# Performance work log

Measured on AMD Instinct MI355X. Metric: run time of the kernel, lower is better.

The kernel has to match this reference:

```python
import jax, jax.numpy as jnp
import numpy as np

VOCAB = 32002        # len(tokenizer) + 2
N_HIDDEN = 512
N_COND = 1024
MAX_LENGTH = 15
BATCH = 256


def setup_inputs() -> dict:
    key = jax.random.key(0)
    ks = jax.random.split(key, 12)
    s = 0.02
    return {
        "caption": jax.random.randint(ks[0], (BATCH, 1), 0, VOCAB, dtype=jnp.int64) if jax.config.jax_enable_x64 else jax.random.randint(ks[0], (BATCH, 1), 0, VOCAB, dtype=jnp.int32),
        "img": jax.random.normal(ks[1], (BATCH, N_COND), dtype=jnp.float32),
        "embedding": jax.random.normal(ks[2], (VOCAB, N_HIDDEN), dtype=jnp.float32) * s,
        "W_cond": jax.random.normal(ks[3], (N_HIDDEN, N_COND), dtype=jnp.float32) * s,
        "b_cond": jnp.zeros((N_HIDDEN,), dtype=jnp.float32),
        "w_ih": jax.random.normal(ks[4], (3 * N_HIDDEN, N_HIDDEN), dtype=jnp.float32) * s,
        "w_hh": jax.random.normal(ks[5], (3 * N_HIDDEN, N_HIDDEN), dtype=jnp.float32) * s,
        "b_ih": jnp.zeros((3 * N_HIDDEN,), dtype=jnp.float32),
        "b_hh": jnp.zeros((3 * N_HIDDEN,), dtype=jnp.float32),
        "W_pred": jax.random.normal(ks[6], (VOCAB, N_HIDDEN), dtype=jnp.float32) * s,
        "b_pred": jnp.zeros((VOCAB,), dtype=jnp.float32),
    }


def gru_cell(x, h, w_ih, w_hh, b_ih, b_hh):
    # PyTorch GRUCell math: gates ordered (reset, update, new)
    gi = x @ w_ih.T + b_ih   # [B, 3H]
    gh = h @ w_hh.T + b_hh   # [B, 3H]
    i_r, i_z, i_n = jnp.split(gi, 3, axis=-1)
    h_r, h_z, h_n = jnp.split(gh, 3, axis=-1)
    r = jax.nn.sigmoid(i_r + h_r)
    z = jax.nn.sigmoid(i_z + h_z)
    n = jnp.tanh(i_n + r * h_n)
    return (1.0 - z) * n + z * h


def reference(caption, img, embedding, W_cond, b_cond, w_ih, w_hh, b_ih, b_hh, W_pred, b_pred):
    h0 = img @ W_cond.T + b_cond           # [B, H] initial GRU hidden state
    tok0 = caption[:, 0].astype(jnp.int32)  # seed token

    def step(carry, _):
        h, tok = carry
        x = embedding[tok]                              # [B, H] gather
        h_new = gru_cell(x, h, w_ih, w_hh, b_ih, b_hh)  # [B, H]
        logits = h_new @ W_pred.T + b_pred              # [B, V]
        nxt = jnp.argmax(logits, axis=-1).astype(jnp.int32)  # top-1 == topk(1)
        return (h_new, nxt), nxt

    (_, _), toks = jax.lax.scan(step, (h0, tok0), None, length=MAX_LENGTH - 1)
    # toks: [T-1, B] -> predictions [B, T] with seed token in column 0
    preds = jnp.concatenate([tok0[:, None], toks.T], axis=1)
    return preds
```

## Files before the change

### kernel.cpp

```cpp
#include <hip/hip_runtime.h>
#include <math.h>

#define BATCH 256
#define NH 512
#define NCOND 1024
#define NV 32002
#define NT 15
#define NVT_F32 501
#define NVT_MF  251

#define SP_P  4096256
#define SP_IH 196608
#define SP_HH 196608
#define SP_C  131072
#define SPLIT_W_BLOCKS 16001
#define SPLIT_S_BLOCKS 2048

typedef short short8 __attribute__((ext_vector_type(8)));
typedef float float4v __attribute__((ext_vector_type(4)));

__device__ __forceinline__ void async_load16(const void* g, void* l){
  __builtin_amdgcn_global_load_lds(
      (const __attribute__((address_space(1))) void*)g,
      (__attribute__((address_space(3))) void*)l, 16, 0, 0);
}

__device__ __forceinline__ void split2(float x, unsigned short& hi, unsigned short& lo){
  unsigned u = __float_as_uint(x);
  unsigned r = u + 0x7fffu + ((u >> 16) & 1u);
  hi = (unsigned short)(r >> 16);
  float fh = __uint_as_float(r & 0xffff0000u);
  float res = x - fh;
  unsigned u2 = __float_as_uint(res);
  unsigned r2 = u2 + 0x7fffu + ((u2 >> 16) & 1u);
  lo = (unsigned short)(r2 >> 16);
}

__device__ __forceinline__ unsigned long long pack_key(float v, int idx){
  unsigned u = __float_as_uint(v);
  u = (u & 0x80000000u) ? ~u : (u | 0x80000000u);
  return ((unsigned long long)u << 32) | (unsigned)(0x7fffffff - idx);
}
__device__ __forceinline__ int key_tok(unsigned long long k){
  return 0x7fffffff - (int)(unsigned)(k & 0xffffffffu);
}

__global__ void k_seed(const int* __restrict__ cap, int* __restrict__ preds){
  int b = threadIdx.x;
  preds[b*NT + 0] = cap[b];
}

__global__ __launch_bounds__(256) void k_split_w(const float* __restrict__ Wp,
    unsigned short* __restrict__ Whi, unsigned short* __restrict__ Wlo){
  size_t i = (size_t)blockIdx.x * 256 + threadIdx.x;
  float4 v = *(const float4*)(Wp + i*4);
  unsigned short h0,l0,h1,l1,h2,l2,h3,l3;
  split2(v.x,h0,l0); split2(v.y,h1,l1); split2(v.z,h2,l2); split2(v.w,h3,l3);
  ushort4 hs = {h0,h1,h2,h3};
  ushort4 ls = {l0,l1,l2,l3};
  *(ushort4*)(Whi + i*4) = hs;
  *(ushort4*)(Wlo + i*4) = ls;
}

__global__ __launch_bounds__(256) void k_split_small(
    const float* __restrict__ wih, const float* __restrict__ whh,
    const float* __restrict__ Wc,
    unsigned short* __restrict__ W6hi, unsigned short* __restrict__ W6lo,
    unsigned short* __restrict__ Wchi, unsigned short* __restrict__ Wclo){
  size_t i = (size_t)blockIdx.x * 256 + threadIdx.x;
  const float* src; unsigned short *dh, *dl; size_t off;
  if (i < SP_IH){ src = wih; dh = W6hi; dl = W6lo; off = i; }
  else if (i < SP_IH + SP_HH){
    src = whh; dh = W6hi + 786432; dl = W6lo + 786432; off = i - SP_IH;
  } else { src = Wc; dh = Wchi; dl = Wclo; off = i - SP_IH - SP_HH; }
  float4 v = *(const float4*)(src + off*4);
  unsigned short h0,l0,h1,l1,h2,l2,h3,l3;
  split2(v.x,h0,l0); split2(v.y,h1,l1); split2(v.z,h2,l2); split2(v.w,h3,l3);
  ushort4 hs = {h0,h1,h2,h3};
  ushort4 ls = {l0,l1,l2,l3};
  *(ushort4*)(dh + off*4) = hs;
  *(ushort4*)(dl + off*4) = ls;
}

__global__ __launch_bounds__(256) void k_h0_mf(
    const float* __restrict__ img,
    const unsigned short* __restrict__ Wchi, const unsigned short* __restrict__ Wclo,
    const float* __restrict__ bc,
    float* __restrict__ h0,
    unsigned short* __restrict__ hhi, unsigned short* __restrict__ hlo){
  __shared__ __align__(16) unsigned short sA[2][16*64];
  __shared__ __align__(16) unsigned short sB[2][64*64];
  int tid = threadIdx.x, w = tid >> 6, lane = tid & 63;
  int jbase = blockIdx.x * 16, bbase = blockIdx.y * 64;
  int r16 = lane & 15, q = lane >> 4;
  float4v acc = {0.f,0.f,0.f,0.f};
  for (int k0 = 0; k0 < NCOND; k0 += 64){
    {
      int arr = w >> 1, t = w & 1;
      int a = t*8 + (lane >> 3);
      int p = (lane & 7) ^ (lane >> 3);
      const unsigned short* gs = (arr ? Wclo : Wchi) + (size_t)(jbase + a)*NCOND + k0 + p*8;
      async_load16(gs, (char*)&sA[arr][0] + t*1024);
    }
    #pragma unroll
    for (int i = 0; i < 2; i++){
      int u = tid + 256*i;
      int b = u >> 3, s = u & 7;
      int p = s ^ (b & 7);
      const float* gp = img + (size_t)(bbase + b)*NCOND + k0 + p*8;
      float4 f0 = *(const float4*)gp, f1 = *(const float4*)(gp + 4);
      short8 hv, lv; unsigned short hh, ll;
      split2(f0.x,hh,ll); hv[0]=(short)hh; lv[0]=(short)ll;
      split2(f0.y,hh,ll); hv[1]=(short)hh; lv[1]=(short)ll;
      split2(f0.z,hh,ll); hv[2]=(short)hh; lv[2]=(short)ll;
      split2(f0.w,hh,ll); hv[3]=(short)hh; lv[3]=(short)ll;
      split2(f1.x,hh,ll); hv[4]=(short)hh; lv[4]=(short)ll;
      split2(f1.y,hh,ll); hv[5]=(short)hh; lv[5]=(short)ll;
      split2(f1.z,hh,ll); hv[6]=(short)hh; lv[6]=(short)ll;
      split2(f1.w,hh,ll); hv[7]=(short)hh; lv[7]=(short)ll;
      *(short8*)((char*)&sB[0][0] + b*128 + s*16) = hv;
      *(short8*)((char*)&sB[1][0] + b*128 + s*16) = lv;
    }
    __syncthreads();
    int rb = w*16 + r16;
    #pragma unroll
    for (int kh = 0; kh < 2; kh++){
      int pa = kh*4 + q;
      int offA = r16*128 + ((pa ^ (r16 & 7))*16);
      int offB = rb*128 + ((pa ^ (rb & 7))*16);
      short8 ah = *(const short8*)((const char*)&sA[0][0] + offA);
      short8 al = *(const short8*)((const char*)&sA[1][0] + offA);
      short8 bh = *(const short8*)((const char*)&sB[0][0] + offB);
      short8 bl = *(const short8*)((const char*)&sB[1][0] + offB);
      acc = __builtin_amdgcn_mfma_f32_16x16x32_bf16(ah, bh, acc, 0,0,0);
      acc = __builtin_amdgcn_mfma_f32_16x16x32_bf16(ah, bl, acc, 0,0,0);
      acc = __builtin_amdgcn_mfma_f32_16x16x32_bf16(al, bh, acc, 0,0,0);
    }
    __syncthreads();
  }
  int b = bbase + w*16 + r16;
  #pragma unroll
  for (int reg = 0; reg < 4; reg++){
    int j = jbase + q*4 + reg;
    float val = acc[reg] + bc[j];
    h0[(size_t)b*NH + j] = val;
    unsigned short sh, sl; split2(val, sh, sl);
    hhi[(size_t)b*NH + j] = sh;
    hlo[(size_t)b*NH + j] = sl;
  }
}

__global__ __launch_bounds__(256) void k_gru_mf(
    const int* __restrict__ cap,
    const unsigned long long* __restrict__ slot_prev,
    const float* __restrict__ emb,
    const unsigned short* __restrict__ W6hi, const unsigned short* __restrict__ W6lo,
    const unsigned short* __restrict__ Hhi, const unsigned short* __restrict__ Hlo,
    const float* __restrict__ bih, const float* __restrict__ bhh,
    const float* __restrict__ hprev, float* __restrict__ hnew,
    unsigned short* __restrict__ nhhi, unsigned short* __restrict__ nhlo,
    int* __restrict__ preds, int use_caption, int pred_col){
  __shared__ __align__(16) unsigned short sAh[96*128];
  __shared__ __align__(16) unsigned short sAl[96*128];
  __shared__ __align__(16) unsigned short sXh[32*128];
  __shared__ __align__(16) unsigned short sXl[32*128];
  __shared__ __align__(16) unsigned short sHh[32*128];
  __shared__ __align__(16) unsigned short sHl[32*128];
  __shared__ float comb[2][768];
  __shared__ int tok[32];
  int tid = threadIdx.x, w = tid >> 6, lane = tid & 63;
  int jbase = blockIdx.x * 16, bbase = blockIdx.y * 32;
  int bsub = w & 1, grp = w >> 1;
  int b16 = lane & 15, q = lane >> 4;

  if (tid < 32){
    int t;
    if (use_caption) t = cap[bbase + tid];
    else {
      t = key_tok(slot_prev[bbase + tid]);
      if (blockIdx.x == 0) preds[(bbase + tid)*NT + pred_col] = t;
    }
    tok[tid] = t;
  }
  __syncthreads();
  int tr0 = tok[tid >> 4];
  int tr1 = tok[16 + (tid >> 4)];

  float4v acc[3];
  #pragma unroll
  for (int g = 0; g < 3; g++) acc[g] = (float4v){0.f,0.f,0.f,0.f};

  for (int k0 = 0; k0 < NH; k0 += 128){
    #pragma unroll
    for (int i = 0; i < 12; i++){
      int idx = w*12 + i;
      int arr = idx >= 24, t = arr ? (idx - 24) : idx;
      int row = t*4 + (lane >> 4);
      int glocal = row >> 4, jr = row & 15;
      int slot = (lane & 15) ^ (row & 15);
      const unsigned short* gs = (arr ? W6lo : W6hi)
          + (size_t)(glocal*512 + jbase + jr)*NH + k0 + slot*8;
      async_load16(gs, (char*)(arr ? sAl : sAh) + t*1024);
    }
    #pragma unroll
    for (int i = 0; i < 4; i++){
      int idx = w*4 + i;
      int arr = idx >= 8, t = idx & 7;
      int row = t*4 + (lane >> 4);
      int slot = (lane & 15) ^ (row & 15);
      const unsigned short* gs = (arr ? Hlo : Hhi)
          + (size_t)(bbase + row)*NH + k0 + slot*8;
      async_load16(gs, (char*)(arr ? sHl : sHh) + t*1024);
    }
    #pragma unroll
    for (int i = 0; i < 2; i++){
      int u = tid + 256*i;
      int row = u >> 4, slot = u & 15;
      int phys = slot ^ (row & 15);
      int tr = i ? tr1 : tr0;
      const float* gp = emb + (size_t)tr*NH + k0 + slot*8;
      float4 f0 = *(const float4*)gp, f1 = *(const float4*)(gp + 4);
      short8 hv, lv; unsigned short hh, ll;
      split2(f0.x,hh,ll); hv[0]=(short)hh; lv[0]=(short)ll;
      split2(f0.y,hh,ll); hv[1]=(short)hh; lv[1]=(short)ll;
      split2(f0.z,hh,ll); hv[2]=(short)hh; lv[2]=(short)ll;
      split2(f0.w,hh,ll); hv[3]=(short)hh; lv[3]=(short)ll;
      split2(f1.x,hh,ll); hv[4]=(short)hh; lv[4]=(short)ll;
      split2(f1.y,hh,ll); hv[5]=(short)hh; lv[5]=(short)ll;
      split2(f1.z,hh,ll); hv[6]=(short)hh; lv[6]=(short)ll;
      split2(f1.w,hh,ll); hv[7]=(short)hh; lv[7]=(short)ll;
      *(short8*)((char*)sXh + row*256 + phys*16) = hv;
      *(short8*)((char*)sXl + row*256 + phys*16) = lv;
    }
    __syncthreads();
    #pragma unroll
    for (int kh = 0; kh < 4; kh++){
      int phys = (kh*4 + q) ^ b16;
      int boff = (bsub*16 + b16)*256 + phys*16;
      short8 bh = grp ? *(const short8*)((const char*)sHh + boff)
                      : *(const short8*)((const char*)sXh + boff);
      short8 bl = grp ? *(const short8*)((const char*)sHl + boff)
                      : *(const short8*)((const char*)sXl + boff);
      #pragma unroll
      for (int gi = 0; gi < 3; gi++){
        int row = (grp*3 + gi)*16 + b16;
        int aoff = row*256 + phys*16;
        short8 ah = *(const short8*)((const char*)sAh + aoff);
        short8 al = *(const short8*)((const char*)sAl + aoff);
        acc[gi] = __builtin_amdgcn_mfma_f32_16x16x32_bf16(ah, bh, acc[gi], 0,0,0);
        acc[gi] = __builtin_amdgcn_mfma_f32_16x16x32_bf16(ah, bl, acc[gi], 0,0,0);
        acc[gi] = __builtin_amdgcn_mfma_f32_16x16x32_bf16(al, bh, acc[gi], 0,0,0);
      }
    }
    __syncthreads();
  }

  if (grp == 1){
    #pragma unroll
    for (int gi = 0; gi < 3; gi++)
      #pragma unroll
      for (int reg = 0; reg < 4; reg++)
        comb[bsub][gi*256 + b16*16 + q*4 + reg] = acc[gi][reg];
  }
  __syncthreads();
  if (grp == 0){
    int b = bbase + bsub*16 + b16;
    #pragma unroll
    for (int reg = 0; reg < 4; reg++){
      int jl = q*4 + reg;
      int j = jbase + jl;
      float hr = comb[bsub][0*256 + b16*16 + jl];
      float hz = comb[bsub][1*256 + b16*16 + jl];
      float hn = comb[bsub][2*256 + b16*16 + jl];
      float gr = acc[0][reg] + hr + bih[j] + bhh[j];
      float gz = acc[1][reg] + hz + bih[j+NH] + bhh[j+NH];
      float in_ = acc[2][reg] + bih[j+2*NH];
      float hn_ = hn + bhh[j+2*NH];
      float r = 1.f/(1.f + expf(-gr));
      float z = 1.f/(1.f + expf(-gz));
      float n = tanhf(in_ + r*hn_);
      float hp = hprev[(size_t)b*NH + j];
      float val = (1.f - z)*n + z*hp;
      hnew[(size_t)b*NH + j] = val;
      unsigned short sh, sl; split2(val, sh, sl);
      nhhi[(size_t)b*NH + j] = sh;
      nhlo[(size_t)b*NH + j] = sl;
    }
  }
}

__global__ __launch_bounds__(256) void k_pred_mf(
    const unsigned short* __restrict__ Hhi, const unsigned short* __restrict__ Hlo,
    const unsigned short* __restrict__ Whi, const unsigned short* __restrict__ Wlo,
    const float* __restrict__ bp,
    unsigned long long* __restrict__ slot){
  __shared__ __align__(16) unsigned short sAh[128*64];
  __shared__ __align__(16) unsigned short sAl[128*64];
  __shared__ __align__(16) unsigned short sBh[128*64];
  __shared__ __align__(16) unsigned short sBl[128*64];
  __shared__ float sval[256];
  __shared__ int   sidx[256];
  int tid = threadIdx.x, w = tid >> 6, lane = tid & 63;
  int vt = blockIdx.x, vbase = vt*128, bbase = blockIdx.y*128;
  int mhalf = w & 1, nhalf = w >> 1;
  unsigned short* mybuf = (w==0)?sAh:(w==1)?sAl:(w==2)?sBh:sBl;
  const unsigned short* gsrc = (w==0)?Whi:(w==1)?Wlo:(w==2)?Hhi:Hlo;
  int rowbase = (w < 2) ? vbase : bbase;
  int isA = (w < 2);
  int rl = lane >> 3, sl = lane & 7;
  int pq = sl ^ rl;
  float4v acc[4][4];
  #pragma unroll
  for (int mi=0;mi<4;mi++)
    #pragma unroll
    for (int ni=0;ni<4;ni++) acc[mi][ni] = (float4v){0.f,0.f,0.f,0.f};
  int q = lane >> 4, b16 = lane & 15;

  for (int k0 = 0; k0 < NH; k0 += 64){
    #pragma unroll
    for (int t = 0; t < 16; t++){
      int grow = rowbase + t*8 + rl;
      if (isA && grow > NV-1) grow = NV-1;
      const unsigned short* gp = gsrc + (size_t)grow*NH + k0 + pq*8;
      async_load16(gp, (char*)mybuf + t*1024);
    }
    __syncthreads();
    #pragma unroll
    for (int kh = 0; kh < 2; kh++){
      int pa = kh*4 + q;
      short8 ah[4], al[4], bh[4], bl[4];
      #pragma unroll
      for (int mi=0;mi<4;mi++){
        int r = mhalf*64 + mi*16 + b16;
        int off = r*128 + ((pa ^ (r & 7))*16);
        ah[mi] = *(const short8*)((const char*)sAh + off);
        al[mi] = *(const short8*)((const char*)sAl + off);
      }
      #pragma unroll
      for (int ni=0;ni<4;ni++){
        int r = nhalf*64 + ni*16 + b16;
        int off = r*128 + ((pa ^ (r & 7))*16);
        bh[ni] = *(const short8*)((const char*)sBh + off);
        bl[ni] = *(const short8*)((const char*)sBl + off);
      }
      #pragma unroll
      for (int mi=0;mi<4;mi++)
        #pragma unroll
        for (int ni=0;ni<4;ni++){
          acc[mi][ni] = __builtin_amdgcn_mfma_f32_16x16x32_bf16(ah[mi], bh[ni], acc[mi][ni], 0,0,0);
          acc[mi][ni] = __builtin_amdgcn_mfma_f32_16x16x32_bf16(ah[mi], bl[ni], acc[mi][ni], 0,0,0);
          acc[mi][ni] = __builtin_amdgcn_mfma_f32_16x16x32_bf16(al[mi], bh[ni], acc[mi][ni], 0,0,0);
        }
    }
    __syncthreads();
  }

  float bestv[4] = {-INFINITY,-INFINITY,-INFINITY,-INFINITY};
  int   besti[4] = {0x7fffffff,0x7fffffff,0x7fffffff,0x7fffffff};
  #pragma unroll
  for (int mi=0;mi<4;mi++){
    #pragma unroll
    for (int reg=0;reg<4;reg++){
      int v = vbase + mhalf*64 + mi*16 + q*4 + reg;
      if (v < NV){
        float bpv = bp[v];
        #pragma unroll
        for (int ni=0;ni<4;ni++){
          float cand = acc[mi][ni][reg] + bpv;
          if (cand > bestv[ni] || (cand == bestv[ni] && v < besti[ni])){
            bestv[ni] = cand; besti[ni] = v;
          }
        }
      }
    }
  }
  #pragma unroll
  for (int ni=0;ni<4;ni++){
    #pragma unroll
    for (int off=16; off<=32; off<<=1){
      float ov = __shfl_xor(bestv[ni], off);
      int   oi = __shfl_xor(besti[ni], off);
      if (ov > bestv[ni] || (ov == bestv[ni] && oi < besti[ni])){
        bestv[ni] = ov; besti[ni] = oi;
      }
    }
    if (lane < 16){
      sval[w*64 + ni*16 + b16] = bestv[ni];
      sidx[w*64 + ni*16 + b16] = besti[ni];
    }
  }
  __syncthreads();
  if (tid < 128){
    int nh = tid >> 6;
    int wA = nh*2, wB = nh*2 + 1;
    int slotid = tid & 63;
    float vA = sval[wA*64 + slotid], vB = sval[wB*64 + slotid];
    int   iA = sidx[wA*64 + slotid], iB = sidx[wB*64 + slotid];
    bool takeB = (vB > vA) || (vB == vA && iB < iA);
    float bv = takeB ? vB : vA;
    int   bi = takeB ? iB : iA;
    atomicMax(slot + bbase + tid, pack_key(bv, bi));
  }
}

__global__ void k_fin_slot(const unsigned long long* __restrict__ slot,
                           int* __restrict__ preds){
  int b = threadIdx.x;
  preds[b*NT + (NT-1)] = key_tok(slot[b]);
}

__global__ __launch_bounds__(256) void k_h0_fb(const float* __restrict__ img,
                                            const float* __restrict__ Wc,
                                            const float* __restrict__ bc,
                                            float* __restrict__ h0){
  __shared__ float As[64*36];
  __shared__ float Bs[64*36];
  int tid = threadIdx.x;
  int tx = tid & 15, ty = tid >> 4;
  int jbase = blockIdx.x * 64;
  int bbase = blockIdx.y * 64;
  int lrow = tid >> 3;
  int lc4  = (tid & 7) << 2;
  float acc[4][4] = {};
  for (int k0 = 0; k0 < NCOND; k0 += 32){
    #pragma unroll
    for (int rr = 0; rr < 64; rr += 32){
      *(float4*)&As[(lrow+rr)*36 + lc4] =
          *(const float4*)(img + (size_t)(bbase+lrow+rr)*NCOND + k0 + lc4);
      *(float4*)&Bs[(lrow+rr)*36 + lc4] =
          *(const float4*)(Wc + (size_t)(jbase+lrow+rr)*NCOND + k0 + lc4);
    }
    __syncthreads();
    #pragma unroll
    for (int kk = 0; kk < 32; kk += 4){
      float4 a[4], w[4];
      #pragma unroll
      for (int i=0;i<4;i++) a[i] = *(float4*)&As[(ty+16*i)*36+kk];
      #pragma unroll
      for (int j=0;j<4;j++) w[j] = *(float4*)&Bs[(tx+16*j)*36+kk];
      #pragma unroll
      for (int i=0;i<4;i++)
        #pragma unroll
        for (int j=0;j<4;j++)
          acc[i][j] += a[i].x*w[j].x + a[i].y*w[j].y + a[i].z*w[j].z + a[i].w*w[j].w;
    }
    __syncthreads();
  }
  #pragma unroll
  for (int i=0;i<4;i++){
    int b = bbase + ty + 16*i;
    #pragma unroll
    for (int j=0;j<4;j++){
      int jj = jbase + tx + 16*j;
      h0[(size_t)b*NH + jj] = acc[i][j] + bc[jj];
    }
  }
}

__global__ __launch_bounds__(256) void k_pred_f32(const float* __restrict__ h,
                                              const float* __restrict__ Wp,
                                              const float* __restrict__ bp,
                                              float* __restrict__ pval,
                                              int* __restrict__ pidx){
  __shared__ float As[64*36];
  __shared__ float Bs[64*36];
  __shared__ float rv[64*16];
  __shared__ int   ri[64*16];
  int tid = threadIdx.x;
  int tx = tid & 15, ty = tid >> 4;
  int vt = blockIdx.x;
  int vbase = vt * 64;
  int bbase = blockIdx.y * 64;
  int lrow = tid >> 3;
  int lc4  = (tid & 7) << 2;
  float acc[4][4] = {};
  for (int k0 = 0; k0 < NH; k0 += 32){
    #pragma unroll
    for (int rr = 0; rr < 64; rr += 32){
      *(float4*)&As[(lrow+rr)*36 + lc4] =
          *(const float4*)(h + (size_t)(bbase+lrow+rr)*NH + k0 + lc4);
      int v = vbase + lrow + rr;
      float4 wv = make_float4(0.f,0.f,0.f,0.f);
      if (v < NV) wv = *(const float4*)(Wp + (size_t)v*NH + k0 + lc4);
      *(float4*)&Bs[(lrow+rr)*36 + lc4] = wv;
    }
    __syncthreads();
    #pragma unroll
    for (int kk = 0; kk < 32; kk += 4){
      float4 a[4], wv[4];
      #pragma unroll
      for (int i=0;i<4;i++) a[i] = *(float4*)&As[(ty+16*i)*36+kk];
      #pragma unroll
      for (int j=0;j<4;j++) wv[j] = *(float4*)&Bs[(tx+16*j)*36+kk];
      #pragma unroll
      for (int i=0;i<4;i++)
        #pragma unroll
        for (int j=0;j<4;j++)
          acc[i][j] += a[i].x*wv[j].x + a[i].y*wv[j].y + a[i].z*wv[j].z + a[i].w*wv[j].w;
    }
    __syncthreads();
  }
  #pragma unroll
  for (int i=0;i<4;i++){
    int bl = ty + 16*i;
    float best = -INFINITY; int bidx = 0;
    #pragma unroll
    for (int j=0;j<4;j++){
      int v = vbase + tx + 16*j;
      if (v < NV){
        float val = acc[i][j] + bp[v];
        if (val > best){ best = val; bidx = v; }
      }
    }
    rv[bl*16+tx] = best; ri[bl*16+tx] = bidx;
  }
  __syncthreads();
  if (tid < 64){
    float best = -INFINITY; int bidx = 0;
    #pragma unroll
    for (int t=0;t<16;t++){
      float v = rv[tid*16+t];
      if (v > best){ best = v; bidx = ri[tid*16+t]; }
    }
    pval[vt*BATCH + bbase + tid] = best;
    pidx[vt*BATCH + bbase + tid] = bidx;
  }
}

__global__ __launch_bounds__(256) void k_gru_fb(const int* __restrict__ cap,
    const float* __restrict__ pval, const int* __restrict__ pidx,
    const float* __restrict__ emb,
    const float* __restrict__ wih, const float* __restrict__ whh,
    const float* __restrict__ bih, const float* __restrict__ bhh,
    const float* __restrict__ hprev, float* __restrict__ hnew,
    int* __restrict__ preds, int use_caption, int pred_col, int nvt){
  __shared__ int   s_tok[32];
  __shared__ float rav[32*8];
  __shared__ int   rai[32*8];
  __shared__ float xs[32*36];
  __shared__ float hs[32*36];
  __shared__ float wis[3*16*36];
  __shared__ float whs[3*16*36];
  int tid = threadIdx.x;
  int tx = tid & 15, ty = tid >> 4;
  int jbase = blockIdx.x * 16;
  int bbase = blockIdx.y * 32;

  if (use_caption){
    if (tid < 32) s_tok[tid] = cap[bbase + tid];
  } else {
    int bl = tid >> 3, l8 = tid & 7;
    float best = -INFINITY; int bidx = 0x7fffffff;
    for (int p = l8; p < nvt; p += 8){
      float v = pval[p*BATCH + bbase + bl];
      int   i = pidx[p*BATCH + bbase + bl];
      if (v > best || (v == best && i < bidx)){ best = v; bidx = i; }
    }
    rav[bl*8 + l8] = best; rai[bl*8 + l8] = bidx;
    __syncthreads();
    if (tid < 32){
      float bb = -INFINITY; int bi = 0x7fffffff;
      #pragma unroll
      for (int t=0;t<8;t++){
        float v = rav[tid*8+t]; int i = rai[tid*8+t];
        if (v > bb || (v == bb && i < bi)){ bb = v; bi = i; }
      }
      s_tok[tid] = bi;
      if (blockIdx.x == 0) preds[(bbase+tid)*NT + pred_col] = bi;
    }
  }
  __syncthreads();

  float acc[2][6] = {};
  int lrow = tid >> 3;
  int lc4  = (tid & 7) << 2;
  for (int k0 = 0; k0 < NH; k0 += 32){
    int tokr = s_tok[lrow];
    *(float4*)&xs[lrow*36 + lc4] =
        *(const float4*)(emb + (size_t)tokr*NH + k0 + lc4);
    *(float4*)&hs[lrow*36 + lc4] =
        *(const float4*)(hprev + (size_t)(bbase+lrow)*NH + k0 + lc4);
    #pragma unroll
    for (int qy = tid; qy < 768; qy += 256){
      int g  = qy >> 7;
      int r  = (qy >> 3) & 15;
      int cc = (qy & 7) << 2;
      const float* wsrc = (g < 3) ? wih : whh;
      int gg = (g < 3) ? g : (g - 3);
      float* dst = (g < 3) ? wis : whs;
      *(float4*)&dst[gg*576 + r*36 + cc] =
          *(const float4*)(wsrc + (size_t)(gg*NH + jbase + r)*NH + k0 + cc);
    }
    __syncthreads();
    #pragma unroll
    for (int kk = 0; kk < 32; kk += 4){
      float4 x0 = *(float4*)&xs[ty*36+kk];
      float4 x1 = *(float4*)&xs[(ty+16)*36+kk];
      float4 h0v = *(float4*)&hs[ty*36+kk];
      float4 h1v = *(float4*)&hs[(ty+16)*36+kk];
      #pragma unroll
      for (int g=0; g<3; g++){
        float4 wi4 = *(float4*)&wis[g*576 + tx*36 + kk];
        float4 wh4 = *(float4*)&whs[g*576 + tx*36 + kk];
        acc[0][g]   += x0.x*wi4.x + x0.y*wi4.y + x0.z*wi4.z + x0.w*wi4.w;
        acc[1][g]   += x1.x*wi4.x + x1.y*wi4.y + x1.z*wi4.z + x1.w*wi4.w;
        acc[0][3+g] += h0v.x*wh4.x + h0v.y*wh4.y + h0v.z*wh4.z + h0v.w*wh4.w;
        acc[1][3+g] += h1v.x*wh4.x + h1v.y*wh4.y + h1v.z*wh4.z + h1v.w*wh4.w;
      }
    }
    __syncthreads();
  }
  int j = jbase + tx;
  float bi_r = bih[j], bi_z = bih[j+NH], bi_n = bih[j+2*NH];
  float bh_r = bhh[j], bh_z = bhh[j+NH], bh_n = bhh[j+2*NH];
  #pragma unroll
  for (int i=0;i<2;i++){
    int b = bbase + ty + 16*i;
    float r = 1.f/(1.f + expf(-((acc[i][0]+bi_r) + (acc[i][3]+bh_r))));
    float z = 1.f/(1.f + expf(-((acc[i][1]+bi_z) + (acc[i][4]+bh_z))));
    float n = tanhf((acc[i][2]+bi_n) + r*(acc[i][5]+bh_n));
    float hp = hprev[(size_t)b*NH + j];
    hnew[(size_t)b*NH + j] = (1.f - z)*n + z*hp;
  }
}

__global__ void k_fin(const float* __restrict__ pval, const int* __restrict__ pidx,
                      int* __restrict__ preds, int col, int nvt){
  __shared__ float rav[32*8];
  __shared__ int   rai[32*8];
  int tid = threadIdx.x;
  int bbase = blockIdx.x * 32;
  int bl = tid >> 3, l8 = tid & 7;
  float best = -INFINITY; int bidx = 0x7fffffff;
  for (int p = l8; p < nvt; p += 8){
    float v = pval[p*BATCH + bbase + bl];
    int   i = pidx[p*BATCH + bbase + bl];
    if (v > best || (v == best && i < bidx)){ best = v; bidx = i; }
  }
  rav[bl*8+l8] = best; rai[bl*8+l8] = bidx;
  __syncthreads();
  if (tid < 32){
    float bb = -INFINITY; int bi = 0x7fffffff;
    #pragma unroll
    for (int t=0;t<8;t++){
      float v = rav[tid*8+t]; int i = rai[tid*8+t];
      if (v > bb || (v == bb && i < bi)){ bb = v; bi = i; }
    }
    preds[(bbase+tid)*NT + col] = bi;
  }
}

extern "C" void kernel_launch(void* const* d_in, const int* in_sizes, int n_in,
                              void* d_out, int out_size, void* d_ws, size_t ws_size,
                              hipStream_t stream){
  const int*   cap = (const int*)d_in[0];
  const float* img = (const float*)d_in[1];
  const float* emb = (const float*)d_in[2];
  const float* Wc  = (const float*)d_in[3];
  const float* bc  = (const float*)d_in[4];
  const float* wih = (const float*)d_in[5];
  const float* whh = (const float*)d_in[6];
  const float* bih = (const float*)d_in[7];
  const float* bhh = (const float*)d_in[8];
  const float* Wp  = (const float*)d_in[9];
  const float* bp  = (const float*)d_in[10];
  int* preds = (int*)d_out;

  char* p = (char*)d_ws;
  float* h0b = (float*)p;                   p += (size_t)BATCH*NH*4;
  float* h1b = (float*)p;                   p += (size_t)BATCH*NH*4;
  float* pval = (float*)p;                  p += (size_t)NVT_F32*BATCH*4;
  int*   pidx = (int*)p;                    p += (size_t)NVT_F32*BATCH*4;
  unsigned short* Hhi0 = (unsigned short*)p; p += (size_t)BATCH*NH*2;
  unsigned short* Hlo0 = (unsigned short*)p; p += (size_t)BATCH*NH*2;
  unsigned short* Hhi1 = (unsigned short*)p; p += (size_t)BATCH*NH*2;
  unsigned short* Hlo1 = (unsigned short*)p; p += (size_t)BATCH*NH*2;
  unsigned short* Whi = (unsigned short*)p;  p += (size_t)NV*NH*2;
  unsigned short* Wlo = (unsigned short*)p;  p += (size_t)NV*NH*2;
  unsigned short* W6hi = (unsigned short*)p; p += (size_t)3072*NH*2;
  unsigned short* W6lo = (unsigned short*)p; p += (size_t)3072*NH*2;
  unsigned short* Wchi = (unsigned short*)p; p += (size_t)NH*NCOND*2;
  unsigned short* Wclo = (unsigned short*)p; p += (size_t)NH*NCOND*2;
  unsigned long long* slots = (unsigned long long*)p; p += (size_t)NT*BATCH*8;
  size_t need = (size_t)(p - (char*)d_ws);

  bool use_mfma = (ws_size >= need);

  k_seed<<<1, 256, 0, stream>>>(cap, preds);
  float* hb[2] = {h0b, h1b};

  if (use_mfma){
    hipMemsetAsync(slots, 0, (size_t)NT*BATCH*8, stream);
    k_split_small<<<dim3(SPLIT_S_BLOCKS), 256, 0, stream>>>(wih, whh, Wc,
                                                            W6hi, W6lo, Wchi, Wclo);
    k_h0_mf<<<dim3(NH/16, BATCH/64), 256, 0, stream>>>(img, Wchi, Wclo, bc,
                                                       h0b, Hhi0, Hlo0);
    unsigned short* Hhs[2] = {Hhi0, Hhi1};
    unsigned short* Hls[2] = {Hlo0, Hlo1};
    k_gru_mf<<<dim3(NH/16, BATCH/32), 256, 0, stream>>>(cap, slots, emb,
        W6hi, W6lo, Hhs[0], Hls[0], bih, bhh,
        hb[0], hb[1], Hhs[1], Hls[1], preds, 1, 0);
    k_split_w<<<dim3(SPLIT_W_BLOCKS), 256, 0, stream>>>(Wp, Whi, Wlo);
    k_pred_mf<<<dim3(NVT_MF, 2), 256, 0, stream>>>(Hhs[1], Hls[1], Whi, Wlo,
                                                   bp, slots + 1*BATCH);
    for (int s = 2; s <= NT-1; s++){
      int pi = (s-1)&1, ci = s&1;
      k_gru_mf<<<dim3(NH/16, BATCH/32), 256, 0, stream>>>(cap, slots + (size_t)(s-1)*BATCH,
          emb, W6hi, W6lo, Hhs[pi], Hls[pi], bih, bhh,
          hb[pi], hb[ci], Hhs[ci], Hls[ci], preds, 0, s-1);
      k_pred_mf<<<dim3(NVT_MF, 2), 256, 0, stream>>>(Hhs[ci], Hls[ci], Whi, Wlo,
                                                     bp, slots + (size_t)s*BATCH);
    }
    k_fin_slot<<<1, 256, 0, stream>>>(slots + (size_t)(NT-1)*BATCH, preds);
  } else {
    k_h0_fb<<<dim3(NH/64, BATCH/64), 256, 0, stream>>>(img, Wc, bc, h0b);
    for (int s = 1; s <= NT-1; s++){
      const float* hprev = hb[(s-1)&1];
      float* hnew = hb[s&1];
      k_gru_fb<<<dim3(NH/16, BATCH/32), 256, 0, stream>>>(cap, pval, pidx, emb, wih, whh,
                                                       bih, bhh, hprev, hnew,
                                                       preds, (s==1)?1:0, s-1, NVT_F32);
      k_pred_f32<<<dim3(NVT_F32, BATCH/64), 256, 0, stream>>>(hnew, Wp, bp, pval, pidx);
    }
    k_fin<<<dim3(BATCH/32), 256, 0, stream>>>(pval, pidx, preds, NT-1, NVT_F32);
  }
}
```

Before: 829.5 us.

## Fuse whole GRU decode into one cooperative persistent kernel with grid barriers

Replaces the chain of roughly 30 kernel launches (weight splitting, h0 projection, per-step GRU and vocab projection) with a single cooperative kernel of 502 blocks that moves between phases using an atomic-counter grid barrier. While the h0 projection runs, the idle blocks split the prediction weights into bf16 hi/lo halves, so that conversion overlaps other work. The GRU tile is reworked to a K-step of 64 with a smaller LDS footprint so it fits the shared 64KB buffer. The aim is to remove launch gaps and per-kernel ramp-up. The cost is spin-wait barriers, and occupancy is capped at two blocks per CU by the 64KB static LDS. The fp32 fallback path is dropped and replaced by the old multi-kernel path, which runs only if the cooperative launch fails.

After: 2.567 ms. 3.09x slower.

```diff
diff --git a/kernel.cpp b/kernel.cpp
--- a/kernel.cpp
+++ b/kernel.cpp
@@ -7,14 +7,14 @@
 #define NV 32002
 #define NT 15
 #define NVT_F32 501
-#define NVT_MF  251
+#define NBLK 502
 
 #define SP_P  4096256
 #define SP_IH 196608
 #define SP_HH 196608
 #define SP_C  131072
-#define SPLIT_W_BLOCKS 16001
-#define SPLIT_S_BLOCKS 2048
+#define SP_SMALL (SP_IH+SP_HH+SP_C)
+#define WP_A  2457600
 
 typedef short short8 __attribute__((ext_vector_type(8)));
 typedef float float4v __attribute__((ext_vector_type(4)));
@@ -45,62 +45,55 @@
   return 0x7fffffff - (int)(unsigned)(k & 0xffffffffu);
 }
 
-__global__ void k_seed(const int* __restrict__ cap, int* __restrict__ preds){
-  int b = threadIdx.x;
-  preds[b*NT + 0] = cap[b];
-}
-
-__global__ __launch_bounds__(256) void k_split_w(const float* __restrict__ Wp,
-    unsigned short* __restrict__ Whi, unsigned short* __restrict__ Wlo){
-  size_t i = (size_t)blockIdx.x * 256 + threadIdx.x;
-  float4 v = *(const float4*)(Wp + i*4);
+__device__ __forceinline__ void gbar(unsigned* cnt, unsigned& target){
+  __syncthreads();
+  if (threadIdx.x == 0){
+    target += NBLK;
+    __hip_atomic_fetch_add(cnt, 1u, __ATOMIC_ACQ_REL, __HIP_MEMORY_SCOPE_AGENT);
+    while (__hip_atomic_load(cnt, __ATOMIC_ACQUIRE, __HIP_MEMORY_SCOPE_AGENT) < target)
+      __builtin_amdgcn_s_sleep(16);
+  }
+  __syncthreads();
+}
+
+__device__ __forceinline__ void split_elem(const float* __restrict__ src,
+    unsigned short* __restrict__ dh, unsigned short* __restrict__ dl, size_t i){
+  float4 v = *(const float4*)(src + i*4);
   unsigned short h0,l0,h1,l1,h2,l2,h3,l3;
   split2(v.x,h0,l0); split2(v.y,h1,l1); split2(v.z,h2,l2); split2(v.w,h3,l3);
   ushort4 hs = {h0,h1,h2,h3};
   ushort4 ls = {l0,l1,l2,l3};
-  *(ushort4*)(Whi + i*4) = hs;
-  *(ushort4*)(Wlo + i*4) = ls;
-}
-
-__global__ __launch_bounds__(256) void k_split_small(
-    const float* __restrict__ wih, const float* __restrict__ whh,
-    const float* __restrict__ Wc,
-    unsigned short* __restrict__ W6hi, unsigned short* __restrict__ W6lo,
-    unsigned short* __restrict__ Wchi, unsigned short* __restrict__ Wclo){
-  size_t i = (size_t)blockIdx.x * 256 + threadIdx.x;
-  const float* src; unsigned short *dh, *dl; size_t off;
-  if (i < SP_IH){ src = wih; dh = W6hi; dl = W6lo; off = i; }
-  else if (i < SP_IH + SP_HH){
-    src = whh; dh = W6hi + 786432; dl = W6lo + 786432; off = i - SP_IH;
-  } else { src = Wc; dh = Wchi; dl = Wclo; off = i - SP_IH - SP_HH; }
-  float4 v = *(const float4*)(src + off*4);
-  unsigned short h0,l0,h1,l1,h2,l2,h3,l3;
-  split2(v.x,h0,l0); split2(v.y,h1,l1); split2(v.z,h2,l2); split2(v.w,h3,l3);
-  ushort4 hs = {h0,h1,h2,h3};
-  ushort4 ls = {l0,l1,l2,l3};
-  *(ushort4*)(dh + off*4) = hs;
-  *(ushort4*)(dl + off*4) = ls;
-}
-
-__global__ __launch_bounds__(256) void k_h0_mf(
+  *(ushort4*)(dh + i*4) = hs;
+  *(ushort4*)(dl + i*4) = ls;
+}
+
+__device__ __forceinline__ void split_small_elem(size_t i,
+    const float* wih, const float* whh, const float* Wc,
+    unsigned short* W6hi, unsigned short* W6lo,
+    unsigned short* Wchi, unsigned short* Wclo){
+  if (i < SP_IH) split_elem(wih, W6hi, W6lo, i);
+  else if (i < SP_IH + SP_HH) split_elem(whh, W6hi + 786432, W6lo + 786432, i - SP_IH);
+  else split_elem(Wc, Wchi, Wclo, i - SP_IH - SP_HH);
+}
+
+__device__ __forceinline__ void phase_h0(char* smem, int blk,
     const float* __restrict__ img,
     const unsigned short* __restrict__ Wchi, const unsigned short* __restrict__ Wclo,
     const float* __restrict__ bc,
     float* __restrict__ h0,
     unsigned short* __restrict__ hhi, unsigned short* __restrict__ hlo){
-  __shared__ __align__(16) unsigned short sA[2][16*64];
-  __shared__ __align__(16) unsigned short sB[2][64*64];
+  char* hA = smem;
+  char* hB = smem + 4096;
   int tid = threadIdx.x, w = tid >> 6, lane = tid & 63;
-  int jbase = blockIdx.x * 16, bbase = blockIdx.y * 64;
+  int jbase = (blk & 31) * 16, bbase = (blk >> 5) * 64;
   int r16 = lane & 15, q = lane >> 4;
   float4v acc = {0.f,0.f,0.f,0.f};
   for (int k0 = 0; k0 < NCOND; k0 += 64){
-    {
-      int arr = w >> 1, t = w & 1;
+    { int arr = w >> 1, t = w & 1;
       int a = t*8 + (lane >> 3);
-      int p = (lane & 7) ^ (lane >> 3);
+      int p = (lane & 7) ^ ((lane >> 3) & 7);
       const unsigned short* gs = (arr ? Wclo : Wchi) + (size_t)(jbase + a)*NCOND + k0 + p*8;
-      async_load16(gs, (char*)&sA[arr][0] + t*1024);
+      async_load16(gs, hA + arr*2048 + t*1024);
     }
     #pragma unroll
     for (int i = 0; i < 2; i++){
@@ -118,8 +111,8 @@
       split2(f1.y,hh,ll); hv[5]=(short)hh; lv[5]=(short)ll;
       split2(f1.z,hh,ll); hv[6]=(short)hh; lv[6]=(short)ll;
       split2(f1.w,hh,ll); hv[7]=(short)hh; lv[7]=(short)ll;
-      *(short8*)((char*)&sB[0][0] + b*128 + s*16) = hv;
-      *(short8*)((char*)&sB[1][0] + b*128 + s*16) = lv;
+      *(short8*)(hB + b*128 + s*16) = hv;
+      *(short8*)(hB + 8192 + b*128 + s*16) = lv;
     }
     __syncthreads();
     int rb = w*16 + r16;
@@ -128,10 +121,10 @@
       int pa = kh*4 + q;
       int offA = r16*128 + ((pa ^ (r16 & 7))*16);
       int offB = rb*128 + ((pa ^ (rb & 7))*16);
-      short8 ah = *(const short8*)((const char*)&sA[0][0] + offA);
-      short8 al = *(const short8*)((const char*)&sA[1][0] + offA);
-      short8 bh = *(const short8*)((const char*)&sB[0][0] + offB);
-      short8 bl = *(const short8*)((const char*)&sB[1][0] + offB);
+      short8 ah = *(const short8*)(hA + offA);
+      short8 al = *(const short8*)(hA + 2048 + offA);
+      short8 bh = *(const short8*)(hB + offB);
+      short8 bl = *(const short8*)(hB + 8192 + offB);
       acc = __builtin_amdgcn_mfma_f32_16x16x32_bf16(ah, bh, acc, 0,0,0);
       acc = __builtin_amdgcn_mfma_f32_16x16x32_bf16(ah, bl, acc, 0,0,0);
       acc = __builtin_amdgcn_mfma_f32_16x16x32_bf16(al, bh, acc, 0,0,0);
@@ -150,9 +143,8 @@
   }
 }
 
-__global__ __launch_bounds__(256) void k_gru_mf(
-    const int* __restrict__ cap,
-    const unsigned long long* __restrict__ slot_prev,
+__device__ __forceinline__ void phase_gru(char* smem, int blk,
+    const int* __restrict__ cap, const unsigned long long* __restrict__ slot_prev,
     const float* __restrict__ emb,
     const unsigned short* __restrict__ W6hi, const unsigned short* __restrict__ W6lo,
     const unsigned short* __restrict__ Hhi, const unsigned short* __restrict__ Hlo,
@@ -160,16 +152,17 @@
     const float* __restrict__ hprev, float* __restrict__ hnew,
     unsigned short* __restrict__ nhhi, unsigned short* __restrict__ nhlo,
     int* __restrict__ preds, int use_caption, int pred_col){
-  __shared__ __align__(16) unsigned short sAh[96*128];
-  __shared__ __align__(16) unsigned short sAl[96*128];
-  __shared__ __align__(16) unsigned short sXh[32*128];
-  __shared__ __align__(16) unsigned short sXl[32*128];
-  __shared__ __align__(16) unsigned short sHh[32*128];
-  __shared__ __align__(16) unsigned short sHl[32*128];
-  __shared__ float comb[2][768];
-  __shared__ int tok[32];
+  char* gAh = smem;
+  char* gAl = smem + 12288;
+  char* gXh = smem + 24576;
+  char* gXl = smem + 28672;
+  char* gHh = smem + 32768;
+  char* gHl = smem + 36864;
+  float* comb = (float*)(smem + 40960);
+  int* tok = (int*)(smem + 47104);
+
   int tid = threadIdx.x, w = tid >> 6, lane = tid & 63;
-  int jbase = blockIdx.x * 16, bbase = blockIdx.y * 32;
+  int jbase = (blk & 31) * 16, bbase = (blk >> 5) * 32;
   int bsub = w & 1, grp = w >> 1;
   int b16 = lane & 15, q = lane >> 4;
 
@@ -178,47 +171,42 @@
     if (use_caption) t = cap[bbase + tid];
     else {
       t = key_tok(slot_prev[bbase + tid]);
-      if (blockIdx.x == 0) preds[(bbase + tid)*NT + pred_col] = t;
+      if ((blk & 31) == 0) preds[(bbase + tid)*NT + pred_col] = t;
     }
     tok[tid] = t;
   }
   __syncthreads();
-  int tr0 = tok[tid >> 4];
-  int tr1 = tok[16 + (tid >> 4)];
 
   float4v acc[3];
   #pragma unroll
   for (int g = 0; g < 3; g++) acc[g] = (float4v){0.f,0.f,0.f,0.f};
 
-  for (int k0 = 0; k0 < NH; k0 += 128){
-    #pragma unroll
-    for (int i = 0; i < 12; i++){
-      int idx = w*12 + i;
-      int arr = idx >= 24, t = arr ? (idx - 24) : idx;
-      int row = t*4 + (lane >> 4);
-      int glocal = row >> 4, jr = row & 15;
-      int slot = (lane & 15) ^ (row & 15);
+  for (int k0 = 0; k0 < NH; k0 += 64){
+    #pragma unroll
+    for (int i = 0; i < 6; i++){
+      int idx = w*6 + i;
+      int arr = idx >= 12, t = arr ? (idx - 12) : idx;
+      int a = t*8 + (lane >> 3);
+      int glocal = a >> 4, jr = a & 15;
+      int p = (lane & 7) ^ ((lane >> 3) & 7);
       const unsigned short* gs = (arr ? W6lo : W6hi)
-          + (size_t)(glocal*512 + jbase + jr)*NH + k0 + slot*8;
-      async_load16(gs, (char*)(arr ? sAl : sAh) + t*1024);
-    }
-    #pragma unroll
-    for (int i = 0; i < 4; i++){
-      int idx = w*4 + i;
-      int arr = idx >= 8, t = idx & 7;
-      int row = t*4 + (lane >> 4);
-      int slot = (lane & 15) ^ (row & 15);
+          + (size_t)(glocal*512 + jbase + jr)*NH + k0 + p*8;
+      async_load16(gs, (arr ? gAl : gAh) + t*1024);
+    }
+    #pragma unroll
+    for (int i = 0; i < 2; i++){
+      int idx = w*2 + i;
+      int arr = idx >> 2, t = idx & 3;
+      int row = t*8 + (lane >> 3);
+      int p = (lane & 7) ^ ((lane >> 3) & 7);
       const unsigned short* gs = (arr ? Hlo : Hhi)
-          + (size_t)(bbase + row)*NH + k0 + slot*8;
-      async_load16(gs, (char*)(arr ? sHl : sHh) + t*1024);
-    }
-    #pragma unroll
-    for (int i = 0; i < 2; i++){
-      int u = tid + 256*i;
-      int row = u >> 4, slot = u & 15;
-      int phys = slot ^ (row & 15);
-      int tr = i ? tr1 : tr0;
-      const float* gp = emb + (size_t)tr*NH + k0 + slot*8;
+          + (size_t)(bbase + row)*NH + k0 + p*8;
+      async_load16(gs, (arr ? gHl : gHh) + t*1024);
+    }
+    {
+      int row = tid >> 3, sl = tid & 7;
+      int p = sl ^ (row & 7);
+      const float* gp = emb + (size_t)tok[row]*NH + k0 + p*8;
       float4 f0 = *(const float4*)gp, f1 = *(const float4*)(gp + 4);
       short8 hv, lv; unsigned short hh, ll;
       split2(f0.x,hh,ll); hv[0]=(short)hh; lv[0]=(short)ll;
@@ -229,24 +217,23 @@
       split2(f1.y,hh,ll); hv[5]=(short)hh; lv[5]=(short)ll;
       split2(f1.z,hh,ll); hv[6]=(short)hh; lv[6]=(short)ll;
       split2(f1.w,hh,ll); hv[7]=(short)hh; lv[7]=(short)ll;
-      *(short8*)((char*)sXh + row*256 + phys*16) = hv;
-      *(short8*)((char*)sXl + row*256 + phys*16) = lv;
+      *(short8*)(gXh + row*128 + sl*16) = hv;
+      *(short8*)(gXl + row*128 + sl*16) = lv;
     }
     __syncthreads();
-    #pragma unroll
-    for (int kh = 0; kh < 4; kh++){
-      int phys = (kh*4 + q) ^ b16;
-      int boff = (bsub*16 + b16)*256 + phys*16;
-      short8 bh = grp ? *(const short8*)((const char*)sHh + boff)
-                      : *(const short8*)((const char*)sXh + boff);
-      short8 bl = grp ? *(const short8*)((const char*)sHl + boff)
-                      : *(const short8*)((const char*)sXl + boff);
+    int rb = bsub*16 + b16;
+    #pragma unroll
+    for (int kh = 0; kh < 2; kh++){
+      int pa = kh*4 + q;
+      int boff = rb*128 + ((pa ^ (rb & 7))*16);
+      short8 bh = grp ? *(const short8*)(gHh + boff) : *(const short8*)(gXh + boff);
+      short8 bl = grp ? *(const short8*)(gHl + boff) : *(const short8*)(gXl + boff);
       #pragma unroll
       for (int gi = 0; gi < 3; gi++){
         int row = (grp*3 + gi)*16 + b16;
-        int aoff = row*256 + phys*16;
-        short8 ah = *(const short8*)((const char*)sAh + aoff);
-        short8 al = *(const short8*)((const char*)sAl + aoff);
+        int aoff = row*128 + ((pa ^ (row & 7))*16);
+        short8 ah = *(const short8*)(gAh + aoff);
+        short8 al = *(const short8*)(gAl + aoff);
         acc[gi] = __builtin_amdgcn_mfma_f32_16x16x32_bf16(ah, bh, acc[gi], 0,0,0);
         acc[gi] = __builtin_amdgcn_mfma_f32_16x16x32_bf16(ah, bl, acc[gi], 0,0,0);
         acc[gi] = __builtin_amdgcn_mfma_f32_16x16x32_bf16(al, bh, acc[gi], 0,0,0);
@@ -260,7 +247,7 @@
     for (int gi = 0; gi < 3; gi++)
       #pragma unroll
       for (int reg = 0; reg < 4; reg++)
-        comb[bsub][gi*256 + b16*16 + q*4 + reg] = acc[gi][reg];
+        comb[bsub*768 + gi*256 + b16*16 + q*4 + reg] = acc[gi][reg];
   }
   __syncthreads();
   if (grp == 0){
@@ -269,9 +256,9 @@
     for (int reg = 0; reg < 4; reg++){
       int jl = q*4 + reg;
       int j = jbase + jl;
-      float hr = comb[bsub][0*256 + b16*16 + jl];
-      float hz = comb[bsub][1*256 + b16*16 + jl];
-      float hn = comb[bsub][2*256 + b16*16 + jl];
+      float hr = comb[bsub*768 + 0*256 + b16*16 + jl];
+      float hz = comb[bsub*768 + 1*256 + b16*16 + jl];
+      float hn = comb[bsub*768 + 2*256 + b16*16 + jl];
       float gr = acc[0][reg] + hr + bih[j] + bhh[j];
       float gz = acc[1][reg] + hz + bih[j+NH] + bhh[j+NH];
       float in_ = acc[2][reg] + bih[j+2*NH];
@@ -289,21 +276,22 @@
   }
 }
 
-__global__ __launch_bounds__(256) void k_pred_mf(
+__device__ __forceinline__ void phase_pred(char* smem, int blk,
     const unsigned short* __restrict__ Hhi, const unsigned short* __restrict__ Hlo,
     const unsigned short* __restrict__ Whi, const unsigned short* __restrict__ Wlo,
     const float* __restrict__ bp,
-    unsigned long long* __restrict__ slot){
-  __shared__ __align__(16) unsigned short sAh[128*64];
-  __shared__ __align__(16) unsigned short sAl[128*64];
-  __shared__ __align__(16) unsigned short sBh[128*64];
-  __shared__ __align__(16) unsigned short sBl[128*64];
-  __shared__ float sval[256];
-  __shared__ int   sidx[256];
+    unsigned long long* __restrict__ slotp){
+  char* sAh = smem;
+  char* sAl = smem + 16384;
+  char* sBh = smem + 32768;
+  char* sBl = smem + 49152;
+  float* sval = (float*)smem;
+  int*   sidx = (int*)(smem + 1024);
+
   int tid = threadIdx.x, w = tid >> 6, lane = tid & 63;
-  int vt = blockIdx.x, vbase = vt*128, bbase = blockIdx.y*128;
+  int vbase = (blk >> 1)*128, bbase = (blk & 1)*128;
   int mhalf = w & 1, nhalf = w >> 1;
-  unsigned short* mybuf = (w==0)?sAh:(w==1)?sAl:(w==2)?sBh:sBl;
+  char* mybuf = (w==0)?sAh:(w==1)?sAl:(w==2)?sBh:sBl;
   const unsigned short* gsrc = (w==0)?Whi:(w==1)?Wlo:(w==2)?Hhi:Hlo;
   int rowbase = (w < 2) ? vbase : bbase;
   int isA = (w < 2);
@@ -322,7 +310,7 @@
       int grow = rowbase + t*8 + rl;
       if (isA && grow > NV-1) grow = NV-1;
       const unsigned short* gp = gsrc + (size_t)grow*NH + k0 + pq*8;
-      async_load16(gp, (char*)mybuf + t*1024);
+      async_load16(gp, mybuf + t*1024);
     }
     __syncthreads();
     #pragma unroll
@@ -333,15 +321,15 @@
       for (int mi=0;mi<4;mi++){
         int r = mhalf*64 + mi*16 + b16;
         int off = r*128 + ((pa ^ (r & 7))*16);
-        ah[mi] = *(const short8*)((const char*)sAh + off);
-        al[mi] = *(const short8*)((const char*)sAl + off);
+        ah[mi] = *(const short8*)(sAh + off);
+        al[mi] = *(const short8*)(sAl + off);
       }
       #pragma unroll
       for (int ni=0;ni<4;ni++){
         int r = nhalf*64 + ni*16 + b16;
         int off = r*128 + ((pa ^ (r & 7))*16);
-        bh[ni] = *(const short8*)((const char*)sBh + off);
-        bl[ni] = *(const short8*)((const char*)sBl + off);
+        bh[ni] = *(const short8*)(sBh + off);
+        bl[ni] = *(const short8*)(sBl + off);
       }
       #pragma unroll
       for (int mi=0;mi<4;mi++)
@@ -393,261 +381,126 @@
   if (tid < 128){
     int nh = tid >> 6;
     int wA = nh*2, wB = nh*2 + 1;
-    int slotid = tid & 63;
-    float vA = sval[wA*64 + slotid], vB = sval[wB*64 + slotid];
-    int   iA = sidx[wA*64 + slotid], iB = sidx[wB*64 + slotid];
+    int so = tid & 63;
+    float vA = sval[wA*64 + so], vB = sval[wB*64 + so];
+    int   iA = sidx[wA*64 + so], iB = sidx[wB*64 + so];
     bool takeB = (vB > vA) || (vB == vA && iB < iA);
-    float bv = takeB ? vB : vA;
-    int   bi = takeB ? iB : iA;
-    atomicMax(slot + bbase + tid, pack_key(bv, bi));
-  }
+    atomicMax(slotp + bbase + tid, pack_key(takeB ? vB : vA, takeB ? iB : iA));
+  }
+}
+
+__global__ __launch_bounds__(256, 2) void k_mega(
+    const int* cap, const float* img, const float* emb,
+    const float* Wc, const float* bc,
+    const float* wih, const float* whh, const float* bih, const float* bhh,
+    const float* Wp, const float* bp,
+    int* preds,
+    float* h0b, float* h1b,
+    unsigned short* Hhi0, unsigned short* Hlo0,
+    unsigned short* Hhi1, unsigned short* Hlo1,
+    unsigned short* Whi, unsigned short* Wlo,
+    unsigned short* W6hi, unsigned short* W6lo,
+    unsigned short* Wchi, unsigned short* Wclo,
+    unsigned long long* slots, unsigned* barcnt)
+{
+  __shared__ __align__(16) char smem[65536];
+  int tid = threadIdx.x, blk = blockIdx.x;
+  unsigned bar_target = 0;
+
+  if (blk == 0) preds[tid*NT] = cap[tid];
+  for (size_t i = (size_t)blk*256 + tid; i < SP_SMALL; i += (size_t)NBLK*256)
+    split_small_elem(i, wih, whh, Wc, W6hi, W6lo, Wchi, Wclo);
+  gbar(barcnt, bar_target);
+
+  if (blk < 128)
+    phase_h0(smem, blk, img, Wchi, Wclo, bc, h0b, Hhi0, Hlo0);
+  else
+    for (size_t i = (size_t)(blk-128)*256 + tid; i < WP_A; i += (size_t)374*256)
+      split_elem(Wp, Whi, Wlo, i);
+  gbar(barcnt, bar_target);
+
+  if (blk < 256)
+    phase_gru(smem, blk, cap, slots, emb, W6hi, W6lo, Hhi0, Hlo0,
+              bih, bhh, h0b, h1b, Hhi1, Hlo1, preds, 1, 0);
+  else
+    for (size_t i = WP_A + (size_t)(blk-256)*256 + tid; i < SP_P; i += (size_t)246*256)
+      split_elem(Wp, Whi, Wlo, i);
+  gbar(barcnt, bar_target);
+
+  unsigned short* Hh[2] = {Hhi0, Hhi1};
+  unsigned short* Hl[2] = {Hlo0, Hlo1};
+  float* hb[2] = {h0b, h1b};
+
+  for (int s = 1; s <= NT-1; s++){
+    phase_pred(smem, blk, Hh[s&1], Hl[s&1], Whi, Wlo, bp, slots + (size_t)s*BATCH);
+    gbar(barcnt, bar_target);
+    if (s < NT-1){
+      if (blk < 256)
+        phase_gru(smem, blk, cap, slots + (size_t)s*BATCH, emb, W6hi, W6lo,
+                  Hh[s&1], Hl[s&1], bih, bhh, hb[s&1], hb[(s+1)&1],
+                  Hh[(s+1)&1], Hl[(s+1)&1], preds, 0, s);
+      gbar(barcnt, bar_target);
+    }
+  }
+  if (blk == 0)
+    preds[tid*NT + (NT-1)] = key_tok(slots[(size_t)(NT-1)*BATCH + tid]);
+}
+
+__global__ void k_seed(const int* __restrict__ cap, int* __restrict__ preds){
+  int b = threadIdx.x;
+  preds[b*NT + 0] = cap[b];
+}
+
+__global__ __launch_bounds__(256) void k_split_w(const float* __restrict__ Wp,
+    unsigned short* __restrict__ Whi, unsigned short* __restrict__ Wlo){
+  size_t i = (size_t)blockIdx.x * 256 + threadIdx.x;
+  if (i < SP_P) split_elem(Wp, Whi, Wlo, i);
+}
+
+__global__ __launch_bounds__(256) void k_split_small(
+    const float* __restrict__ wih, const float* __restrict__ whh,
+    const float* __restrict__ Wc,
+    unsigned short* __restrict__ W6hi, unsigned short* __restrict__ W6lo,
+    unsigned short* __restrict__ Wchi, unsigned short* __restrict__ Wclo){
+  size_t i = (size_t)blockIdx.x * 256 + threadIdx.x;
+  if (i < SP_SMALL) split_small_elem(i, wih, whh, Wc, W6hi, W6lo, Wchi, Wclo);
+}
+
+__global__ __launch_bounds__(256) void k_h0_mf(
+    const float* __restrict__ img,
+    const unsigned short* __restrict__ Wchi, const unsigned short* __restrict__ Wclo,
+    const float* __restrict__ bc, float* __restrict__ h0,
+    unsigned short* __restrict__ hhi, unsigned short* __restrict__ hlo){
+  __shared__ __align__(16) char smem[20480];
+  phase_h0(smem, blockIdx.x, img, Wchi, Wclo, bc, h0, hhi, hlo);
+}
+
+__global__ __launch_bounds__(256) void k_gru_mf(
+    const int* __restrict__ cap, const unsigned long long* __restrict__ slot_prev,
+    const float* __restrict__ emb,
+    const unsigned short* __restrict__ W6hi, const unsigned short* __restrict__ W6lo,
+    const unsigned short* __restrict__ Hhi, const unsigned short* __restrict__ Hlo,
+    const float* __restrict__ bih, const float* __restrict__ bhh,
+    const float* __restrict__ hprev, float* __restrict__ hnew,
+    unsigned short* __restrict__ nhhi, unsigned short* __restrict__ nhlo,
+    int* __restrict__ preds, int use_caption, int pred_col){
+  __shared__ __align__(16) char smem[47232];
+  phase_gru(smem, blockIdx.x, cap, slot_prev, emb, W6hi, W6lo, Hhi, Hlo,
+            bih, bhh, hprev, hnew, nhhi, nhlo, preds, use_caption, pred_col);
+}
+
+__global__ __launch_bounds__(256) void k_pred_mf(
+    const unsigned short* __restrict__ Hhi, const unsigned short* __restrict__ Hlo,
+    const unsigned short* __restrict__ Whi, const unsigned short* __restrict__ Wlo,
+    const float* __restrict__ bp, unsigned long long* __restrict__ slotp){
+  __shared__ __align__(16) char smem[65536];
+  phase_pred(smem, blockIdx.x, Hhi, Hlo, Whi, Wlo, bp, slotp);
 }
 
 __global__ void k_fin_slot(const unsigned long long* __restrict__ slot,
                            int* __restrict__ preds){
   int b = threadIdx.x;
   preds[b*NT + (NT-1)] = key_tok(slot[b]);
-}
-
-__global__ __launch_bounds__(256) void k_h0_fb(const float* __restrict__ img,
-                                            const float* __restrict__ Wc,
-                                            const float* __restrict__ bc,
-                                            float* __restrict__ h0){
-  __shared__ float As[64*36];
-  __shared__ float Bs[64*36];
-  int tid = threadIdx.x;
-  int tx = tid & 15, ty = tid >> 4;
-  int jbase = blockIdx.x * 64;
-  int bbase = blockIdx.y * 64;
-  int lrow = tid >> 3;
-  int lc4  = (tid & 7) << 2;
-  float acc[4][4] = {};
-  for (int k0 = 0; k0 < NCOND; k0 += 32){
-    #pragma unroll
-    for (int rr = 0; rr < 64; rr += 32){
-      *(float4*)&As[(lrow+rr)*36 + lc4] =
-          *(const float4*)(img + (size_t)(bbase+lrow+rr)*NCOND + k0 + lc4);
-      *(float4*)&Bs[(lrow+rr)*36 + lc4] =
-          *(const float4*)(Wc + (size_t)(jbase+lrow+rr)*NCOND + k0 + lc4);
-    }
-    __syncthreads();
-    #pragma unroll
-    for (int kk = 0; kk < 32; kk += 4){
-      float4 a[4], w[4];
-      #pragma unroll
-      for (int i=0;i<4;i++) a[i] = *(float4*)&As[(ty+16*i)*36+kk];
-      #pragma unroll
-      for (int j=0;j<4;j++) w[j] = *(float4*)&Bs[(tx+16*j)*36+kk];
-      #pragma unroll
-      for (int i=0;i<4;i++)
-        #pragma unroll
-        for (int j=0;j<4;j++)
-          acc[i][j] += a[i].x*w[j].x + a[i].y*w[j].y + a[i].z*w[j].z + a[i].w*w[j].w;
-    }
-    __syncthreads();
-  }
-  #pragma unroll
-  for (int i=0;i<4;i++){
-    int b = bbase + ty + 16*i;
-    #pragma unroll
-    for (int j=0;j<4;j++){
-      int jj = jbase + tx + 16*j;
-      h0[(size_t)b*NH + jj] = acc[i][j] + bc[jj];
-    }
-  }
-}
-
-__global__ __launch_bounds__(256) void k_pred_f32(const float* __restrict__ h,
-                                              const float* __restrict__ Wp,
-                                              const float* __restrict__ bp,
-                                              float* __restrict__ pval,
-                                              int* __restrict__ pidx){
-  __shared__ float As[64*36];
-  __shared__ float Bs[64*36];
-  __shared__ float rv[64*16];
-  __shared__ int   ri[64*16];
-  int tid = threadIdx.x;
-  int tx = tid & 15, ty = tid >> 4;
-  int vt = blockIdx.x;
-  int vbase = vt * 64;
-  int bbase = blockIdx.y * 64;
-  int lrow = tid >> 3;
-  int lc4  = (tid & 7) << 2;
-  float acc[4][4] = {};
-  for (int k0 = 0; k0 < NH; k0 += 32){
-    #pragma unroll
-    for (int rr = 0; rr < 64; rr += 32){
-      *(float4*)&As[(lrow+rr)*36 + lc4] =
-          *(const float4*)(h + (size_t)(bbase+lrow+rr)*NH + k0 + lc4);
-      int v = vbase + lrow + rr;
-      float4 wv = make_float4(0.f,0.f,0.f,0.f);
-      if (v < NV) wv = *(const float4*)(Wp + (size_t)v*NH + k0 + lc4);
-      *(float4*)&Bs[(lrow+rr)*36 + lc4] = wv;
-    }
-    __syncthreads();
-    #pragma unroll
-    for (int kk = 0; kk < 32; kk += 4){
-      float4 a[4], wv[4];
-      #pragma unroll
-      for (int i=0;i<4;i++) a[i] = *(float4*)&As[(ty+16*i)*36+kk];
-      #pragma unroll
-      for (int j=0;j<4;j++) wv[j] = *(float4*)&Bs[(tx+16*j)*36+kk];
-      #pragma unroll
-      for (int i=0;i<4;i++)
-        #pragma unroll
-        for (int j=0;j<4;j++)
-          acc[i][j] += a[i].x*wv[j].x + a[i].y*wv[j].y + a[i].z*wv[j].z + a[i].w*wv[j].w;
-    }
-    __syncthreads();
-  }
-  #pragma unroll
-  for (int i=0;i<4;i++){
-    int bl = ty + 16*i;
-    float best = -INFINITY; int bidx = 0;
-    #pragma unroll
-    for (int j=0;j<4;j++){
-      int v = vbase + tx + 16*j;
-      if (v < NV){
-        float val = acc[i][j] + bp[v];
-        if (val > best){ best = val; bidx = v; }
-      }
-    }
-    rv[bl*16+tx] = best; ri[bl*16+tx] = bidx;
-  }
-  __syncthreads();
-  if (tid < 64){
-    float best = -INFINITY; int bidx = 0;
-    #pragma unroll
-    for (int t=0;t<16;t++){
-      float v = rv[tid*16+t];
-      if (v > best){ best = v; bidx = ri[tid*16+t]; }
-    }
-    pval[vt*BATCH + bbase + tid] = best;
-    pidx[vt*BATCH + bbase + tid] = bidx;
-  }
-}
-
-__global__ __launch_bounds__(256) void k_gru_fb(const int* __restrict__ cap,
-    const float* __restrict__ pval, const int* __restrict__ pidx,
-    const float* __restrict__ emb,
-    const float* __restrict__ wih, const float* __restrict__ whh,
-    const float* __restrict__ bih, const float* __restrict__ bhh,
-    const float* __restrict__ hprev, float* __restrict__ hnew,
-    int* __restrict__ preds, int use_caption, int pred_col, int nvt){
-  __shared__ int   s_tok[32];
-  __shared__ float rav[32*8];
-  __shared__ int   rai[32*8];
-  __shared__ float xs[32*36];
-  __shared__ float hs[32*36];
-  __shared__ float wis[3*16*36];
-  __shared__ float whs[3*16*36];
-  int tid = threadIdx.x;
-  int tx = tid & 15, ty = tid >> 4;
-  int jbase = blockIdx.x * 16;
-  int bbase = blockIdx.y * 32;
-
-  if (use_caption){
-    if (tid < 32) s_tok[tid] = cap[bbase + tid];
-  } else {
-    int bl = tid >> 3, l8 = tid & 7;
-    float best = -INFINITY; int bidx = 0x7fffffff;
-    for (int p = l8; p < nvt; p += 8){
-      float v = pval[p*BATCH + bbase + bl];
-      int   i = pidx[p*BATCH + bbase + bl];
-      if (v > best || (v == best && i < bidx)){ best = v; bidx = i; }
-    }
-    rav[bl*8 + l8] = best; rai[bl*8 + l8] = bidx;
-    __syncthreads();
-    if (tid < 32){
-      float bb = -INFINITY; int bi = 0x7fffffff;
-      #pragma unroll
-      for (int t=0;t<8;t++){
-        float v = rav[tid*8+t]; int i = rai[tid*8+t];
-        if (v > bb || (v == bb && i < bi)){ bb = v; bi = i; }
-      }
-      s_tok[tid] = bi;
-      if (blockIdx.x == 0) preds[(bbase+tid)*NT + pred_col] = bi;
-    }
-  }
-  __syncthreads();
-
-  float acc[2][6] = {};
-  int lrow = tid >> 3;
-  int lc4  = (tid & 7) << 2;
-  for (int k0 = 0; k0 < NH; k0 += 32){
-    int tokr = s_tok[lrow];
-    *(float4*)&xs[lrow*36 + lc4] =
-        *(const float4*)(emb + (size_t)tokr*NH + k0 + lc4);
-    *(float4*)&hs[lrow*36 + lc4] =
-        *(const float4*)(hprev + (size_t)(bbase+lrow)*NH + k0 + lc4);
-    #pragma unroll
-    for (int qy = tid; qy < 768; qy += 256){
-      int g  = qy >> 7;
-      int r  = (qy >> 3) & 15;
-      int cc = (qy & 7) << 2;
-      const float* wsrc = (g < 3) ? wih : whh;
-      int gg = (g < 3) ? g : (g - 3);
-      float* dst = (g < 3) ? wis : whs;
-      *(float4*)&dst[gg*576 + r*36 + cc] =
-          *(const float4*)(wsrc + (size_t)(gg*NH + jbase + r)*NH + k0 + cc);
-    }
-    __syncthreads();
-    #pragma unroll
-    for (int kk = 0; kk < 32; kk += 4){
-      float4 x0 = *(float4*)&xs[ty*36+kk];
-      float4 x1 = *(float4*)&xs[(ty+16)*36+kk];
-      float4 h0v = *(float4*)&hs[ty*36+kk];
-      float4 h1v = *(float4*)&hs[(ty+16)*36+kk];
-      #pragma unroll
-      for (int g=0; g<3; g++){
-        float4 wi4 = *(float4*)&wis[g*576 + tx*36 + kk];
-        float4 wh4 = *(float4*)&whs[g*576 + tx*36 + kk];
-        acc[0][g]   += x0.x*wi4.x + x0.y*wi4.y + x0.z*wi4.z + x0.w*wi4.w;
-        acc[1][g]   += x1.x*wi4.x + x1.y*wi4.y + x1.z*wi4.z + x1.w*wi4.w;
-        acc[0][3+g] += h0v.x*wh4.x + h0v.y*wh4.y + h0v.z*wh4.z + h0v.w*wh4.w;
-        acc[1][3+g] += h1v.x*wh4.x + h1v.y*wh4.y + h1v.z*wh4.z + h1v.w*wh4.w;
-      }
-    }
-    __syncthreads();
-  }
-  int j = jbase + tx;
-  float bi_r = bih[j], bi_z = bih[j+NH], bi_n = bih[j+2*NH];
-  float bh_r = bhh[j], bh_z = bhh[j+NH], bh_n = bhh[j+2*NH];
-  #pragma unroll
-  for (int i=0;i<2;i++){
-    int b = bbase + ty + 16*i;
-    float r = 1.f/(1.f + expf(-((acc[i][0]+bi_r) + (acc[i][3]+bh_r))));
-    float z = 1.f/(1.f + expf(-((acc[i][1]+bi_z) + (acc[i][4]+bh_z))));
-    float n = tanhf((acc[i][2]+bi_n) + r*(acc[i][5]+bh_n));
-    float hp = hprev[(size_t)b*NH + j];
-    hnew[(size_t)b*NH + j] = (1.f - z)*n + z*hp;
-  }
-}
-
-__global__ void k_fin(const float* __restrict__ pval, const int* __restrict__ pidx,
-                      int* __restrict__ preds, int col, int nvt){
-  __shared__ float rav[32*8];
-  __shared__ int   rai[32*8];
-  int tid = threadIdx.x;
-  int bbase = blockIdx.x * 32;
-  int bl = tid >> 3, l8 = tid & 7;
-  float best = -INFINITY; int bidx = 0x7fffffff;
-  for (int p = l8; p < nvt; p += 8){
-    float v = pval[p*BATCH + bbase + bl];
-    int   i = pidx[p*BATCH + bbase + bl];
-    if (v > best || (v == best && i < bidx)){ best = v; bidx = i; }
-  }
-  rav[bl*8+l8] = best; rai[bl*8+l8] = bidx;
-  __syncthreads();
-  if (tid < 32){
-    float bb = -INFINITY; int bi = 0x7fffffff;
-    #pragma unroll
-    for (int t=0;t<8;t++){
-      float v = rav[tid*8+t]; int i = rai[tid*8+t];
-      if (v > bb || (v == bb && i < bi)){ bb = v; bi = i; }
-    }
-    preds[(bbase+tid)*NT + col] = bi;
-  }
 }
 
 extern "C" void kernel_launch(void* const* d_in, const int* in_sizes, int n_in,
@@ -669,8 +522,6 @@
   char* p = (char*)d_ws;
   float* h0b = (float*)p;                   p += (size_t)BATCH*NH*4;
   float* h1b = (float*)p;                   p += (size_t)BATCH*NH*4;
-  float* pval = (float*)p;                  p += (size_t)NVT_F32*BATCH*4;
-  int*   pidx = (int*)p;                    p += (size_t)NVT_F32*BATCH*4;
   unsigned short* Hhi0 = (unsigned short*)p; p += (size_t)BATCH*NH*2;
   unsigned short* Hlo0 = (unsigned short*)p; p += (size_t)BATCH*NH*2;
   unsigned short* Hhi1 = (unsigned short*)p; p += (size_t)BATCH*NH*2;
@@ -682,46 +533,42 @@
   unsigned short* Wchi = (unsigned short*)p; p += (size_t)NH*NCOND*2;
   unsigned short* Wclo = (unsigned short*)p; p += (size_t)NH*NCOND*2;
   unsigned long long* slots = (unsigned long long*)p; p += (size_t)NT*BATCH*8;
-  size_t need = (size_t)(p - (char*)d_ws);
-
-  bool use_mfma = (ws_size >= need);
-
-  k_seed<<<1, 256, 0, stream>>>(cap, preds);
-  float* hb[2] = {h0b, h1b};
-
-  if (use_mfma){
-    hipMemsetAsync(slots, 0, (size_t)NT*BATCH*8, stream);
-    k_split_small<<<dim3(SPLIT_S_BLOCKS), 256, 0, stream>>>(wih, whh, Wc,
-                                                            W6hi, W6lo, Wchi, Wclo);
-    k_h0_mf<<<dim3(NH/16, BATCH/64), 256, 0, stream>>>(img, Wchi, Wclo, bc,
-                                                       h0b, Hhi0, Hlo0);
-    unsigned short* Hhs[2] = {Hhi0, Hhi1};
-    unsigned short* Hls[2] = {Hlo0, Hlo1};
-    k_gru_mf<<<dim3(NH/16, BATCH/32), 256, 0, stream>>>(cap, slots, emb,
-        W6hi, W6lo, Hhs[0], Hls[0], bih, bhh,
-        hb[0], hb[1], Hhs[1], Hls[1], preds, 1, 0);
-    k_split_w<<<dim3(SPLIT_W_BLOCKS), 256, 0, stream>>>(Wp, Whi, Wlo);
-    k_pred_mf<<<dim3(NVT_MF, 2), 256, 0, stream>>>(Hhs[1], Hls[1], Whi, Wlo,
-                                                   bp, slots + 1*BATCH);
+  unsigned* barcnt = (unsigned*)p;           p += 64;
+
+  hipMemsetAsync(barcnt, 0, 4, stream);
+  hipMemsetAsync(slots, 0, (size_t)NT*BATCH*8, stream);
+
+  void* args[] = {
+    (void*)&cap, (void*)&img, (void*)&emb, (void*)&Wc, (void*)&bc,
+    (void*)&wih, (void*)&whh, (void*)&bih, (void*)&bhh, (void*)&Wp, (void*)&bp,
+    (void*)&preds, (void*)&h0b, (void*)&h1b,
+    (void*)&Hhi0, (void*)&Hlo0, (void*)&Hhi1, (void*)&Hlo1,
+    (void*)&Whi, (void*)&Wlo, (void*)&W6hi, (void*)&W6lo,
+    (void*)&Wchi, (void*)&Wclo, (void*)&slots, (void*)&barcnt
+  };
+  hipError_t err = hipLaunchCooperativeKernel((const void*)k_mega, dim3(NBLK),
+                                              dim3(256), args, 0, stream);
+  if (err != hipSuccess){
+    k_seed<<<1, 256, 0, stream>>>(cap, preds);
+    k_split_small<<<dim3(SP_SMALL/256), 256, 0, stream>>>(wih, whh, Wc,
+                                                          W6hi, W6lo, Wchi, Wclo);
+    k_h0_mf<<<dim3(128), 256, 0, stream>>>(img, Wchi, Wclo, bc, h0b, Hhi0, Hlo0);
+    unsigned short* Hh[2] = {Hhi0, Hhi1};
+    unsigned short* Hl[2] = {Hlo0, Hlo1};
+    float* hb[2] = {h0b, h1b};
+    k_gru_mf<<<dim3(256), 256, 0, stream>>>(cap, slots, emb, W6hi, W6lo,
+        Hh[0], Hl[0], bih, bhh, hb[0], hb[1], Hh[1], Hl[1], preds, 1, 0);
+    k_split_w<<<dim3(SP_P/256), 256, 0, stream>>>(Wp, Whi, Wlo);
+    k_pred_mf<<<dim3(NBLK), 256, 0, stream>>>(Hh[1], Hl[1], Whi, Wlo, bp,
+                                              slots + 1*BATCH);
     for (int s = 2; s <= NT-1; s++){
       int pi = (s-1)&1, ci = s&1;
-      k_gru_mf<<<dim3(NH/16, BATCH/32), 256, 0, stream>>>(cap, slots + (size_t)(s-1)*BATCH,
-          emb, W6hi, W6lo, Hhs[pi], Hls[pi], bih, bhh,
-          hb[pi], hb[ci], Hhs[ci], Hls[ci], preds, 0, s-1);
-      k_pred_mf<<<dim3(NVT_MF, 2), 256, 0, stream>>>(Hhs[ci], Hls[ci], Whi, Wlo,
-                                                     bp, slots + (size_t)s*BATCH);
+      k_gru_mf<<<dim3(256), 256, 0, stream>>>(cap, slots + (size_t)(s-1)*BATCH,
+          emb, W6hi, W6lo, Hh[pi], Hl[pi], bih, bhh,
+          hb[pi], hb[ci], Hh[ci], Hl[ci], preds, 0, s-1);
+      k_pred_mf<<<dim3(NBLK), 256, 0, stream>>>(Hh[ci], Hl[ci], Whi, Wlo, bp,
+                                                slots + (size_t)s*BATCH);
     }
     k_fin_slot<<<1, 256, 0, stream>>>(slots + (size_t)(NT-1)*BATCH, preds);
-  } else {
-    k_h0_fb<<<dim3(NH/64, BATCH/64), 256, 0, stream>>>(img, Wc, bc, h0b);
-    for (int s = 1; s <= NT-1; s++){
-      const float* hprev = hb[(s-1)&1];
-      float* hnew = hb[s&1];
-      k_gru_fb<<<dim3(NH/16, BATCH/32), 256, 0, stream>>>(cap, pval, pidx, emb, wih, whh,
-                                                       bih, bhh, hprev, hnew,
-                                                       preds, (s==1)?1:0, s-1, NVT_F32);
-      k_pred_f32<<<dim3(NVT_F32, BATCH/64), 256, 0, stream>>>(hnew, Wp, bp, pval, pidx);
-    }
-    k_fin<<<dim3(BATCH/32), 256, 0, stream>>>(pval, pidx, preds, NT-1, NVT_F32);
-  }
-}
+  }
+}
```
